# Performance work log

Measured on AMD Instinct MI355X. Metric: run time of the kernel, lower is better.

Reference implementation:

```python
import jax, jax.numpy as jnp
import numpy as np

N_NODES = 100_000
N_EDGES = 3_200_000
EPS_BN = 1e-5
EPS_NORM = 1e-12


def _sage_conv(x, src, dst, ew, pw, pb, lw, lb, rw, n_nodes):
    # project=True: relu(Linear_in->in) applied to source features
    xp = jax.nn.relu(x @ pw + pb)                       # [N, in]
    msg = xp[src] * ew[:, None]                         # [E, in] gather + weight
    agg = jax.ops.segment_sum(msg, dst, num_segments=n_nodes)      # scatter-sum
    cnt = jax.ops.segment_sum(jnp.ones_like(ew), dst, num_segments=n_nodes)
    mean = agg / jnp.maximum(cnt, 1.0)[:, None]         # scatter-mean
    out = mean @ lw + lb + x @ rw                       # neighbor lin + root lin
    # normalize=True: L2 normalize rows
    nrm = jnp.sqrt(jnp.sum(out * out, axis=-1, keepdims=True))
    return out / jnp.maximum(nrm, EPS_NORM)


def setup_inputs() -> dict:
    key = jax.random.key(0)
    ks = jax.random.split(key, 20)
    d = {}
    d["h"] = jax.random.normal(ks[0], (N_NODES, 5), dtype=jnp.float32)
    d["edge_index"] = jax.random.randint(ks[1], (2, N_EDGES), 0, N_NODES, dtype=jnp.int32)
    d["edge_weight"] = jax.random.uniform(ks[2], (N_EDGES,), dtype=jnp.float32)
    # BatchNorm1d(5) params (conv2_norm in the source is unused in forward)
    d["bn_gamma"] = jnp.ones((5,), jnp.float32)
    d["bn_beta"] = jnp.zeros((5,), jnp.float32)

    def lin(k, fan_in, fan_out):
        return jax.random.normal(k, (fan_in, fan_out), jnp.float32) * (1.0 / np.sqrt(fan_in))

    # conv1: 5 -> 64 ; conv2: 64 -> 64 (fixing source bug) ; conv3: 64 -> 5
    dims = [(5, 64), (64, 64), (64, 5)]
    ki = 3
    for i, (fi, fo) in enumerate(dims, start=1):
        d[f"c{i}_pw"] = lin(ks[ki], fi, fi); ki += 1
        d[f"c{i}_pb"] = jnp.zeros((fi,), jnp.float32)
        d[f"c{i}_lw"] = lin(ks[ki], fi, fo); ki += 1
        d[f"c{i}_lb"] = jnp.zeros((fo,), jnp.float32)
        d[f"c{i}_rw"] = lin(ks[ki], fi, fo); ki += 1
    return d


def reference(h, edge_index, edge_weight, bn_gamma, bn_beta,
              c1_pw, c1_pb, c1_lw, c1_lb, c1_rw,
              c2_pw, c2_pb, c2_lw, c2_lb, c2_rw,
              c3_pw, c3_pb, c3_lw, c3_lb, c3_rw):
    src, dst = edge_index[0], edge_index[1]
    # BatchNorm1d (training-mode batch statistics, biased variance)
    mu = jnp.mean(h, axis=0)
    var = jnp.mean((h - mu) ** 2, axis=0)
    x = (h - mu) * jax.lax.rsqrt(var + EPS_BN) * bn_gamma + bn_beta

    x = jax.nn.relu(_sage_conv(x, src, dst, edge_weight, c1_pw, c1_pb, c1_lw, c1_lb, c1_rw, N_NODES))
    x = jax.nn.relu(_sage_conv(x, src, dst, edge_weight, c2_pw, c2_pb, c2_lw, c2_lb, c2_rw, N_NODES))
    x = _sage_conv(x, src, dst, edge_weight, c3_pw, c3_pb, c3_lw, c3_lb, c3_rw, N_NODES)
    # dropout omitted (deterministic / eval-mode reference)
    return x
```

## Files before the change

### kernel.cpp

```cpp
#include <hip/hip_runtime.h>
#include <hip/hip_bf16.h>

#define N_NODES 100000
#define N_EDGES 3200000
#define BSH 8
#define NB 391

typedef __hip_bfloat16 bf16;

#define RL(v, k) __int_as_float(__builtin_amdgcn_readlane(__float_as_int(v), (k)))

__device__ __forceinline__ float loadF(const void* p, long long i, int isf32) {
    if (isf32) return ((const float*)p)[i];
    unsigned short v = ((const unsigned short*)p)[i];
    union { unsigned u; float f; } c;
    c.u = ((unsigned)v) << 16;
    return c.f;
}

__device__ __forceinline__ unsigned packEdge(int s, float w) {
    bf16 b = __float2bfloat16(w);
    unsigned short bits = *(unsigned short*)&b;
    return ((unsigned)s << 15) | (unsigned)(bits & 0x7FFF);
}
__device__ __forceinline__ int edgeSrc(unsigned u) { return (int)(u >> 15); }
__device__ __forceinline__ float edgeW(unsigned u) {
    union { unsigned x; float f; } c;
    c.x = (u & 0x7FFFu) << 16;
    return c.f;
}

#define W_GAMMA 0
#define W_BETA 8
#define W_C1PW 16
#define W_C1PB 48
#define W_C1LW 56
#define W_C1LB 376
#define W_C1RW 440
#define W_C2PW 760
#define W_C2PB 4856
#define W_C2LW 4920
#define W_C2LB 9016
#define W_C2RW 9080
#define W_C3PW 13176
#define W_C3PB 17272
#define W_C3LW 17336
#define W_C3LB 17656
#define W_C3RW 17664

__global__ void detect_dtype(const void* ew, int* flag) {
    const unsigned short* u = (const unsigned short*)ew;
    int lane = threadIdx.x;
    int big = 0;
    for (int i = lane; i < 1024; i += 64) {
        unsigned short v = u[2 * i];
        int ex = (v >> 7) & 0xFF;
        if (ex >= 128) big++;
    }
#pragma unroll
    for (int o = 32; o; o >>= 1) big += __shfl_xor(big, o, 64);
    if (lane == 0) *flag = (big > 100) ? 1 : 0;
}

__global__ void cvt_weights(const int* flag,
                            const void* p0, const void* p1, const void* p2, const void* p3,
                            const void* p4, const void* p5, const void* p6, const void* p7,
                            const void* p8, const void* p9, const void* p10, const void* p11,
                            const void* p12, const void* p13, const void* p14, const void* p15,
                            const void* p16, float* __restrict__ wts) {
    const void* ptrs[17] = {p0, p1, p2, p3, p4, p5, p6, p7, p8,
                            p9, p10, p11, p12, p13, p14, p15, p16};
    const int sz[17] = {5, 5, 25, 5, 320, 64, 320, 4096, 64,
                        4096, 64, 4096, 4096, 64, 320, 5, 320};
    const int off[17] = {W_GAMMA, W_BETA, W_C1PW, W_C1PB, W_C1LW, W_C1LB, W_C1RW,
                         W_C2PW, W_C2PB, W_C2LW, W_C2LB, W_C2RW,
                         W_C3PW, W_C3PB, W_C3LW, W_C3LB, W_C3RW};
    int t = blockIdx.x;
    int isf32 = *flag;
    for (int i = threadIdx.x; i < sz[t]; i += blockDim.x)
        wts[off[t] + i] = loadF(ptrs[t], i, isf32);
}

__global__ void bn_stats(const void* __restrict__ h, const int* __restrict__ flag,
                         float* __restrict__ stats) {
    int isf32 = *flag;
    float s[5] = {0, 0, 0, 0, 0}, q[5] = {0, 0, 0, 0, 0};
    int tid = blockIdx.x * blockDim.x + threadIdx.x;
    int stride = gridDim.x * blockDim.x;
    for (int i = tid; i < N_NODES; i += stride) {
#pragma unroll
        for (int f = 0; f < 5; f++) {
            float v = loadF(h, i * 5 + f, isf32);
            s[f] += v;
            q[f] += v * v;
        }
    }
#pragma unroll
    for (int f = 0; f < 5; f++) {
#pragma unroll
        for (int o = 32; o; o >>= 1) {
            s[f] += __shfl_xor(s[f], o, 64);
            q[f] += __shfl_xor(q[f], o, 64);
        }
    }
    __shared__ float ls[4][10];
    int wave = threadIdx.x >> 6, lane = threadIdx.x & 63;
    if (lane == 0) {
#pragma unroll
        for (int f = 0; f < 5; f++) { ls[wave][f] = s[f]; ls[wave][5 + f] = q[f]; }
    }
    __syncthreads();
    if (threadIdx.x < 10) {
        float v = ls[0][threadIdx.x] + ls[1][threadIdx.x] + ls[2][threadIdx.x] + ls[3][threadIdx.x];
        int idx = (threadIdx.x < 5) ? threadIdx.x : (threadIdx.x - 5 + 8);
        atomicAdd(&stats[idx], v);
    }
}

__global__ void bn_proj1(const void* __restrict__ h, const int* __restrict__ flag,
                         const float* __restrict__ stats, const float* __restrict__ wts,
                         float* __restrict__ xbn, float* __restrict__ xp1) {
    __shared__ float s_sc[5], s_sb[5];
    if (threadIdx.x < 5) {
        int f = threadIdx.x;
        float mean = stats[f] / (float)N_NODES;
        float var = stats[8 + f] / (float)N_NODES - mean * mean;
        float sc = wts[W_GAMMA + f] * rsqrtf(var + 1e-5f);
        s_sc[f] = sc;
        s_sb[f] = wts[W_BETA + f] - mean * sc;
    }
    __syncthreads();
    int isf32 = *flag;
    int i = blockIdx.x * blockDim.x + threadIdx.x;
    if (i >= N_NODES) return;
    float x[5];
#pragma unroll
    for (int f = 0; f < 5; f++)
        x[f] = loadF(h, i * 5 + f, isf32) * s_sc[f] + s_sb[f];
#pragma unroll
    for (int f = 0; f < 5; f++) xbn[i * 5 + f] = x[f];
#pragma unroll
    for (int j = 0; j < 5; j++) {
        float a = wts[W_C1PB + j];
#pragma unroll
        for (int k = 0; k < 5; k++) a += x[k] * wts[W_C1PW + k * 5 + j];
        xp1[i * 8 + j] = fmaxf(a, 0.f);
    }
#pragma unroll
    for (int j = 5; j < 8; j++) xp1[i * 8 + j] = 0.f;
}

__global__ void __launch_bounds__(256) bucket_hist(const int* __restrict__ dst,
                                                   int* __restrict__ bucketCnt) {
    __shared__ int hcnt[NB];
    for (int i = threadIdx.x; i < NB; i += 256) hcnt[i] = 0;
    __syncthreads();
    int per = (N_EDGES + gridDim.x - 1) / gridDim.x;
    int s = blockIdx.x * per;
    int e = min(s + per, N_EDGES);
    for (int i = s + threadIdx.x; i < e; i += 256)
        atomicAdd(&hcnt[dst[i] >> BSH], 1);
    __syncthreads();
    for (int i = threadIdx.x; i < NB; i += 256)
        if (hcnt[i]) atomicAdd(&bucketCnt[i], hcnt[i]);
}

__global__ void __launch_bounds__(512) bucket_scan(const int* __restrict__ bucketCnt,
                                                   int* __restrict__ bucketStart,
                                                   int* __restrict__ bucketCursor) {
    int tid = threadIdx.x, lane = tid & 63, w = tid >> 6;
    int v = (tid < NB) ? bucketCnt[tid] : 0;
    int sc = v;
#pragma unroll
    for (int o = 1; o < 64; o <<= 1) {
        int t = __shfl_up(sc, o, 64);
        if (lane >= o) sc += t;
    }
    __shared__ int ws[8];
    if (lane == 63) ws[w] = sc;
    __syncthreads();
    if (w == 0) {
        int wv = (lane < 8) ? ws[lane] : 0;
        int s2 = wv;
#pragma unroll
        for (int o = 1; o < 8; o <<= 1) {
            int t = __shfl_up(s2, o, 64);
            if (lane >= o) s2 += t;
        }
        if (lane < 8) ws[lane] = s2;
    }
    __syncthreads();
    int woff = w ? ws[w - 1] : 0;
    int ex = woff + sc - v;
    if (tid < NB) {
        bucketStart[tid] = ex;
        bucketCursor[tid] = ex;
    }
    if (tid == 0) bucketStart[NB] = N_EDGES;
}

__global__ void __launch_bounds__(256) bucket_stage(const int* __restrict__ src,
                                                    const int* __restrict__ dst,
                                                    const void* __restrict__ ew,
                                                    const int* __restrict__ flag,
                                                    int* __restrict__ bucketCursor,
                                                    uint2* __restrict__ stage) {
    __shared__ int hcnt[NB], cur[NB];
    int isf32 = *flag;
    for (int i = threadIdx.x; i < NB; i += 256) hcnt[i] = 0;
    __syncthreads();
    int per = (N_EDGES + gridDim.x - 1) / gridDim.x;
    int s = blockIdx.x * per;
    int e = min(s + per, N_EDGES);
    for (int i = s + threadIdx.x; i < e; i += 256)
        atomicAdd(&hcnt[dst[i] >> BSH], 1);
    __syncthreads();
    for (int i = threadIdx.x; i < NB; i += 256)
        cur[i] = hcnt[i] ? atomicAdd(&bucketCursor[i], hcnt[i]) : 0;
    __syncthreads();
    for (int i = s + threadIdx.x; i < e; i += 256) {
        int d = dst[i];
        int slot = atomicAdd(&cur[d >> BSH], 1);
        stage[slot] = make_uint2((unsigned)d, packEdge(src[i], loadF(ew, i, isf32)));
    }
}

__global__ void __launch_bounds__(256) bucket_place(const uint2* __restrict__ stage,
                                                    const int* __restrict__ bucketStart,
                                                    int* __restrict__ start,
                                                    unsigned* __restrict__ perm) {
    int b = blockIdx.x, tid = threadIdx.x;
    int base = bucketStart[b];
    int cnt = bucketStart[b + 1] - base;
    int n0 = b << BSH;
    int nn = min(256, N_NODES - n0);
    __shared__ int lcnt[256], loff[256], ws[4];
    lcnt[tid] = 0;
    __syncthreads();
    for (int i = tid; i < cnt; i += 256)
        atomicAdd(&lcnt[stage[base + i].x & 255], 1);
    __syncthreads();
    int lane = tid & 63, w = tid >> 6;
    int v = lcnt[tid];
    int sc = v;
#pragma unroll
    for (int o = 1; o < 64; o <<= 1) {
        int t = __shfl_up(sc, o, 64);
        if (lane >= o) sc += t;
    }
    if (lane == 63) ws[w] = sc;
    __syncthreads();
    int woff = 0;
    for (int k = 0; k < w; k++) woff += ws[k];
    loff[tid] = woff + sc - v;
    __syncthreads();
    if (tid < nn) start[n0 + tid] = base + loff[tid];
    if (b == 0 && tid == 0) start[N_NODES] = N_EDGES;
    lcnt[tid] = 0;
    __syncthreads();
    for (int i = tid; i < cnt; i += 256) {
        uint2 sv = stage[base + i];
        int l = sv.x & 255;
        int p = atomicAdd(&lcnt[l], 1);
        perm[base + loff[l] + p] = sv.y;
    }
}

__global__ void __launch_bounds__(256) conv1_gather(const float* __restrict__ xp1,
                                                    const float* __restrict__ xbn,
                                                    const int* __restrict__ start,
                                                    const unsigned* __restrict__ perm,
                                                    const float* __restrict__ wts,
                                                    float* __restrict__ x1) {
    int lane = threadIdx.x & 63;
    int slot = lane >> 3, f = lane & 7;
    int wid = __builtin_amdgcn_readfirstlane((blockIdx.x * blockDim.x + threadIdx.x) >> 6);
    int nw = (gridDim.x * blockDim.x) >> 6;
    float Wlw[5], Wrw[5];
#pragma unroll
    for (int k = 0; k < 5; k++) {
        Wlw[k] = wts[W_C1LW + k * 64 + lane];
        Wrw[k] = wts[W_C1RW + k * 64 + lane];
    }
    float lb = wts[W_C1LB + lane];
    for (int node = wid; node < N_NODES; node += nw) {
        int e0 = start[node], e1 = start[node + 1];
        float acc = 0.f;
        for (int eb = e0; eb < e1; eb += 32) {
            unsigned p[4];
#pragma unroll
            for (int q = 0; q < 4; q++) {
                int e = eb + q * 8 + slot;
                p[q] = (e < e1) ? perm[e] : 0u;
            }
            float v[4];
#pragma unroll
            for (int q = 0; q < 4; q++)
                v[q] = xp1[(size_t)(p[q] >> 15) * 8 + f];
#pragma unroll
            for (int q = 0; q < 4; q++)
                acc += v[q] * edgeW(p[q]);
        }
        acc += __shfl_xor(acc, 8, 64);
        acc += __shfl_xor(acc, 16, 64);
        acc += __shfl_xor(acc, 32, 64);
        float ic = 1.f / fmaxf((float)(e1 - e0), 1.f);
        float xb = (lane < 5) ? xbn[node * 5 + lane] : 0.f;
        float out = lb;
#pragma unroll
        for (int k = 0; k < 5; k++)
            out += RL(acc, k) * ic * Wlw[k] + RL(xb, k) * Wrw[k];
        float ss = out * out;
#pragma unroll
        for (int o = 32; o; o >>= 1) ss += __shfl_xor(ss, o, 64);
        float xv = fmaxf(out / fmaxf(sqrtf(ss), 1e-12f), 0.f);
        x1[(size_t)node * 64 + lane] = xv;
    }
}

__global__ void __launch_bounds__(256) proj2_blocked(const float* __restrict__ x1,
                                                     const float* __restrict__ wts,
                                                     bf16* __restrict__ y2) {
    int lane = threadIdx.x & 63;
    int wid = (blockIdx.x * blockDim.x + threadIdx.x) >> 6;
    int nb = wid * 16;
    if (nb >= N_NODES) return;
    float xv[16];
#pragma unroll
    for (int n = 0; n < 16; n++) {
        int node = nb + n;
        xv[n] = (node < N_NODES) ? x1[(size_t)node * 64 + lane] : 0.f;
    }
    float a[16];
    float pb = wts[W_C2PB + lane];
#pragma unroll
    for (int n = 0; n < 16; n++) a[n] = pb;
#pragma unroll
    for (int c = 0; c < 4; c++) {
        float Wc[16];
#pragma unroll
        for (int j = 0; j < 16; j++) Wc[j] = wts[W_C2PW + (c * 16 + j) * 64 + lane];
#pragma unroll
        for (int n = 0; n < 16; n++) {
#pragma unroll
            for (int j = 0; j < 16; j++)
                a[n] += RL(xv[n], c * 16 + j) * Wc[j];
        }
    }
#pragma unroll
    for (int n = 0; n < 16; n++) a[n] = fmaxf(a[n], 0.f);
    float b[16];
#pragma unroll
    for (int n = 0; n < 16; n++) b[n] = 0.f;
#pragma unroll
    for (int c = 0; c < 4; c++) {
        float Wc[16];
#pragma unroll
        for (int j = 0; j < 16; j++) Wc[j] = wts[W_C2LW + (c * 16 + j) * 64 + lane];
#pragma unroll
        for (int n = 0; n < 16; n++) {
#pragma unroll
            for (int j = 0; j < 16; j++)
                b[n] += RL(a[n], c * 16 + j) * Wc[j];
        }
    }
#pragma unroll
    for (int n = 0; n < 16; n++) {
        int node = nb + n;
        if (node < N_NODES) y2[(size_t)node * 64 + lane] = __float2bfloat16(b[n]);
    }
}

__global__ void __launch_bounds__(256) conv2_fused_reg(const bf16* __restrict__ y2,
                                                       const int* __restrict__ start,
                                                       const unsigned* __restrict__ perm,
                                                       const float* __restrict__ x1,
                                                       const float* __restrict__ wts,
                                                       float* __restrict__ x2) {
    int lane = threadIdx.x & 63;
    int wid = __builtin_amdgcn_readfirstlane((blockIdx.x * blockDim.x + threadIdx.x) >> 6);
    int nw = (gridDim.x * blockDim.x) >> 6;
    float W[64];
#pragma unroll
    for (int k = 0; k < 64; k++) W[k] = wts[W_C2RW + k * 64 + lane];
    float lb = wts[W_C2LB + lane];
    for (int node = wid; node < N_NODES; node += nw) {
        int e0 = start[node], e1 = start[node + 1];
        float acc = 0.f;
        int e = e0;
        for (; e + 16 <= e1; e += 16) {
            unsigned p[16];
#pragma unroll
            for (int u = 0; u < 16; u++) p[u] = perm[e + u];
            float v[16];
#pragma unroll
            for (int u = 0; u < 16; u++)
                v[u] = __bfloat162float(y2[(size_t)edgeSrc(p[u]) * 64 + lane]);
#pragma unroll
            for (int u = 0; u < 16; u++) acc += v[u] * edgeW(p[u]);
        }
        for (; e + 4 <= e1; e += 4) {
            unsigned p[4];
#pragma unroll
            for (int u = 0; u < 4; u++) p[u] = perm[e + u];
            float v[4];
#pragma unroll
            for (int u = 0; u < 4; u++)
                v[u] = __bfloat162float(y2[(size_t)edgeSrc(p[u]) * 64 + lane]);
#pragma unroll
            for (int u = 0; u < 4; u++) acc += v[u] * edgeW(p[u]);
        }
        for (; e < e1; e++) {
            unsigned p = perm[e];
            acc += __bfloat162float(y2[(size_t)edgeSrc(p) * 64 + lane]) * edgeW(p);
        }
        float ic = 1.f / fmaxf((float)(e1 - e0), 1.f);
        float xv = x1[(size_t)node * 64 + lane];
        float o0 = acc * ic + lb, o1 = 0.f, o2 = 0.f, o3 = 0.f;
#pragma unroll
        for (int k = 0; k < 64; k += 4) {
            o0 += RL(xv, k) * W[k];
            o1 += RL(xv, k + 1) * W[k + 1];
            o2 += RL(xv, k + 2) * W[k + 2];
            o3 += RL(xv, k + 3) * W[k + 3];
        }
        float out = (o0 + o1) + (o2 + o3);
        float ss = out * out;
#pragma unroll
        for (int o = 32; o; o >>= 1) ss += __shfl_xor(ss, o, 64);
        float v = out / fmaxf(sqrtf(ss), 1e-12f);
        x2[(size_t)node * 64 + lane] = fmaxf(v, 0.f);
    }
}

__global__ void __launch_bounds__(256) proj3_reg(const float* __restrict__ x2,
                                                 const float* __restrict__ wts,
                                                 float* __restrict__ y3) {
    int lane = threadIdx.x & 63;
    int wid = __builtin_amdgcn_readfirstlane((blockIdx.x * blockDim.x + threadIdx.x) >> 6);
    int nw = (gridDim.x * blockDim.x) >> 6;
    float W1[64], Wl[5];
#pragma unroll
    for (int k = 0; k < 64; k++) W1[k] = wts[W_C3PW + k * 64 + lane];
#pragma unroll
    for (int j = 0; j < 5; j++) Wl[j] = wts[W_C3LW + lane * 5 + j];
    float pb = wts[W_C3PB + lane];
    for (int node = wid; node < N_NODES; node += nw) {
        float xv = x2[(size_t)node * 64 + lane];
        float a0 = pb, a1 = 0.f, a2 = 0.f, a3 = 0.f;
#pragma unroll
        for (int k = 0; k < 64; k += 4) {
            a0 += RL(xv, k) * W1[k];
            a1 += RL(xv, k + 1) * W1[k + 1];
            a2 += RL(xv, k + 2) * W1[k + 2];
            a3 += RL(xv, k + 3) * W1[k + 3];
        }
        float xp = fmaxf((a0 + a1) + (a2 + a3), 0.f);
#pragma unroll
        for (int j = 0; j < 5; j++) {
            float p = xp * Wl[j];
#pragma unroll
            for (int o = 32; o; o >>= 1) p += __shfl_xor(p, o, 64);
            if (lane == j) y3[(size_t)node * 8 + j] = p;
        }
    }
}

__global__ void __launch_bounds__(256) conv3_fused(const float* __restrict__ y3,
                                                   const float* __restrict__ x2,
                                                   const int* __restrict__ start,
                                                   const unsigned* __restrict__ perm,
                                                   const float* __restrict__ wts,
                                                   const int* __restrict__ flag,
                                                   void* __restrict__ outp) {
    int lane = threadIdx.x & 63;
    int wid = __builtin_amdgcn_readfirstlane((blockIdx.x * blockDim.x + threadIdx.x) >> 6);
    int nw = (gridDim.x * blockDim.x) >> 6;
    float Wr[5];
#pragma unroll
    for (int j = 0; j < 5; j++) Wr[j] = wts[W_C3RW + lane * 5 + j];
    float lb3[5];
#pragma unroll
    for (int j = 0; j < 5; j++) lb3[j] = wts[W_C3LB + j];
    int isf32 = *flag;
    for (int node = wid; node < N_NODES; node += nw) {
        int e0 = start[node], e1 = start[node + 1];
        float s0 = 0, s1 = 0, s2 = 0, s3 = 0, s4 = 0;
        for (int eb = e0; eb < e1; eb += 64) {
            int e = eb + lane;
            if (e < e1) {
                unsigned p = perm[e];
                float w = edgeW(p);
                const float* row = y3 + (size_t)edgeSrc(p) * 8;
                float4 v4 = *(const float4*)row;
                float v5 = row[4];
                s0 += v4.x * w; s1 += v4.y * w; s2 += v4.z * w;
                s3 += v4.w * w; s4 += v5 * w;
            }
        }
#pragma unroll
        for (int o = 32; o; o >>= 1) {
            s0 += __shfl_xor(s0, o, 64);
            s1 += __shfl_xor(s1, o, 64);
            s2 += __shfl_xor(s2, o, 64);
            s3 += __shfl_xor(s3, o, 64);
            s4 += __shfl_xor(s4, o, 64);
        }
        float ic = 1.f / fmaxf((float)(e1 - e0), 1.f);
        float xv = x2[(size_t)node * 64 + lane];
        float m[5] = {s0 * ic, s1 * ic, s2 * ic, s3 * ic, s4 * ic};
        float r[5], ss = 0.f;
#pragma unroll
        for (int j = 0; j < 5; j++) {
            float p = xv * Wr[j];
#pragma unroll
            for (int o = 32; o; o >>= 1) p += __shfl_xor(p, o, 64);
            r[j] = p + m[j] + lb3[j];
            ss += r[j] * r[j];
        }
        float inv = 1.f / fmaxf(sqrtf(ss), 1e-12f);
#pragma unroll
        for (int j = 0; j < 5; j++) {
            if (lane == j) {
                float v = r[j] * inv;
                if (isf32) ((float*)outp)[node * 5 + j] = v;
                else ((bf16*)outp)[node * 5 + j] = __float2bfloat16(v);
            }
        }
    }
}

extern "C" void kernel_launch(void* const* d_in, const int* in_sizes, int n_in,
                              void* d_out, int out_size, void* d_ws, size_t ws_size,
                              hipStream_t stream) {
    const void* h = d_in[0];
    const int* ei = (const int*)d_in[1];
    const int* src = ei;
    const int* dst = ei + N_EDGES;
    const void* ew = d_in[2];

    float* W = (float*)d_ws;
    int* flag = (int*)W;
    float* stats = W + 16;
    float* wts = W + 64;
    float* xbn = W + 20480;
    float* xp1 = xbn + N_NODES * 5;
    int* startp = (int*)(xp1 + N_NODES * 8);
    int* bucketCnt = startp + N_NODES + 64;
    int* bucketStart = bucketCnt + NB + 1;
    int* bucketCursor = bucketStart + NB + 1;
    unsigned* perm = (unsigned*)(bucketCursor + NB + 62);
    float* x1 = (float*)(perm + N_EDGES);
    uint2* stage = (uint2*)x1;
    bf16* y2 = (bf16*)(x1 + (size_t)N_NODES * 64);
    float* x2 = x1;
    float* y3 = xp1;

    detect_dtype<<<1, 64, 0, stream>>>(ew, flag);
    cvt_weights<<<17, 256, 0, stream>>>(flag,
        d_in[3], d_in[4],
        d_in[5], d_in[6], d_in[7], d_in[8], d_in[9],
        d_in[10], d_in[11], d_in[12], d_in[13], d_in[14],
        d_in[15], d_in[16], d_in[17], d_in[18], d_in[19],
        wts);

    hipMemsetAsync(stats, 0, 32 * sizeof(float), stream);
    hipMemsetAsync(bucketCnt, 0, NB * sizeof(int), stream);

    bn_stats<<<200, 256, 0, stream>>>(h, flag, stats);
    bn_proj1<<<(N_NODES + 255) / 256, 256, 0, stream>>>(h, flag, stats, wts, xbn, xp1);

    bucket_hist<<<512, 256, 0, stream>>>(dst, bucketCnt);
    bucket_scan<<<1, 512, 0, stream>>>(bucketCnt, bucketStart, bucketCursor);
    bucket_stage<<<512, 256, 0, stream>>>(src, dst, ew, flag, bucketCursor, stage);
    bucket_place<<<NB, 256, 0, stream>>>(stage, bucketStart, startp, perm);

    conv1_gather<<<4096, 256, 0, stream>>>(xp1, xbn, startp, perm, wts, x1);
    proj2_blocked<<<(N_NODES / 16 + 1 + 3) / 4, 256, 0, stream>>>(x1, wts, y2);

    conv2_fused_reg<<<4096, 256, 0, stream>>>(y2, startp, perm, x1, wts, x2);

    proj3_reg<<<2048, 256, 0, stream>>>(x2, wts, y3);
    conv3_fused<<<2048, 256, 0, stream>>>(y3, x2, startp, perm, wts, flag, d_out);
}
```

Measured before the change: 558.9 us.

## Sort edges by source and gather conv2 in source-range phases with grid barriers

Adds a kernel that bitonic-sorts each node's packed edge list by source index and records per-node boundaries for four source-ID quarters. The conv2 gather then runs as a persistent-style kernel of 1024 blocks that process one source quarter at a time, separated by global atomic spin barriers, accumulating partial sums in shared memory. The goal is to keep the working set of y2 rows cache-resident during each phase and so cut random-gather traffic. The cost is an extra sort pass, grid-wide barriers that depend on all blocks being co-resident (there is a timeout fallback), and lower occupancy from the launch bounds and shared-memory use.

```diff
diff --git a/kernel.cpp b/kernel.cpp
--- a/kernel.cpp
+++ b/kernel.cpp
@@ -5,6 +5,8 @@
 #define N_EDGES 3200000
 #define BSH 8
 #define NB 391
+#define CNBLK 1024
+#define NPB 100
 
 typedef __hip_bfloat16 bf16;
 
@@ -266,6 +268,46 @@
     }
 }
 
+__global__ void __launch_bounds__(256) sort_perm(const int* __restrict__ start,
+                                                 unsigned* __restrict__ perm,
+                                                 ushort4* __restrict__ cums) {
+    int lane = threadIdx.x & 63;
+    int wid = (blockIdx.x * blockDim.x + threadIdx.x) >> 6;
+    int nw = (gridDim.x * blockDim.x) >> 6;
+    for (int node = wid; node < N_NODES; node += nw) {
+        int e0 = start[node], e1 = start[node + 1];
+        int deg = e1 - e0;
+        if (deg > 64) {
+            if (lane == 0)
+                cums[node] = make_ushort4((unsigned short)deg, (unsigned short)deg,
+                                          (unsigned short)deg, (unsigned short)deg);
+            continue;
+        }
+        unsigned v = (lane < deg) ? perm[e0 + lane] : 0xFFFFFFFFu;
+#pragma unroll
+        for (int k = 2; k <= 64; k <<= 1) {
+#pragma unroll
+            for (int j = k >> 1; j > 0; j >>= 1) {
+                unsigned o = __shfl_xor(v, j, 64);
+                bool asc = ((lane & k) == 0);
+                bool lower = ((lane & j) == 0);
+                unsigned mn = min(v, o), mx = max(v, o);
+                v = (asc == lower) ? mn : mx;
+            }
+        }
+        if (lane < deg) perm[e0 + lane] = v;
+        int srcn = (int)(v >> 15);
+        bool valid = (lane < deg);
+        int ph = (srcn >= 25000) + (srcn >= 50000) + (srcn >= 75000);
+        unsigned long long b0 = __ballot(valid && ph <= 0);
+        unsigned long long b1 = __ballot(valid && ph <= 1);
+        unsigned long long b2 = __ballot(valid && ph <= 2);
+        if (lane == 0)
+            cums[node] = make_ushort4((unsigned short)__popcll(b0), (unsigned short)__popcll(b1),
+                                      (unsigned short)__popcll(b2), (unsigned short)deg);
+    }
+}
+
 __global__ void __launch_bounds__(256) conv1_gather(const float* __restrict__ xp1,
                                                     const float* __restrict__ xbn,
                                                     const int* __restrict__ start,
@@ -371,50 +413,75 @@
     }
 }
 
-__global__ void __launch_bounds__(256) conv2_fused_reg(const bf16* __restrict__ y2,
-                                                       const int* __restrict__ start,
-                                                       const unsigned* __restrict__ perm,
-                                                       const float* __restrict__ x1,
-                                                       const float* __restrict__ wts,
-                                                       float* __restrict__ x2) {
-    int lane = threadIdx.x & 63;
-    int wid = __builtin_amdgcn_readfirstlane((blockIdx.x * blockDim.x + threadIdx.x) >> 6);
-    int nw = (gridDim.x * blockDim.x) >> 6;
+__global__ void __launch_bounds__(256, 4) conv2_coop(const bf16* __restrict__ y2,
+                                                     const int* __restrict__ start,
+                                                     const unsigned* __restrict__ perm,
+                                                     const ushort4* __restrict__ cums,
+                                                     const float* __restrict__ x1,
+                                                     const float* __restrict__ wts,
+                                                     float* __restrict__ x2,
+                                                     int* __restrict__ bar) {
+    __shared__ float sacc[NPB * 64];
+    int tid = threadIdx.x, lane = tid & 63, w = tid >> 6;
+    int nb0 = blockIdx.x * NPB;
+    for (int i = tid; i < NPB * 64; i += 256) sacc[i] = 0.f;
+    __syncthreads();
+#pragma unroll
+    for (int p = 0; p < 4; p++) {
+        for (int i = w; i < NPB; i += 4) {
+            int node = nb0 + i;
+            if (node >= N_NODES) break;
+            int e0 = start[node];
+            ushort4 c = cums[node];
+            int lo = (p == 0) ? 0 : ((p == 1) ? c.x : ((p == 2) ? c.y : c.z));
+            int hi = (p == 0) ? c.x : ((p == 1) ? c.y : ((p == 2) ? c.z : c.w));
+            int e = e0 + lo, eh = e0 + hi;
+            float a = 0.f;
+            for (; e + 8 <= eh; e += 8) {
+                unsigned pk[8];
+#pragma unroll
+                for (int u = 0; u < 8; u++) pk[u] = perm[e + u];
+                float vv[8];
+#pragma unroll
+                for (int u = 0; u < 8; u++)
+                    vv[u] = __bfloat162float(y2[(size_t)(pk[u] >> 15) * 64 + lane]);
+#pragma unroll
+                for (int u = 0; u < 8; u++) a += vv[u] * edgeW(pk[u]);
+            }
+            for (; e + 2 <= eh; e += 2) {
+                unsigned pa = perm[e], pb2 = perm[e + 1];
+                float va = __bfloat162float(y2[(size_t)(pa >> 15) * 64 + lane]);
+                float vb = __bfloat162float(y2[(size_t)(pb2 >> 15) * 64 + lane]);
+                a += va * edgeW(pa) + vb * edgeW(pb2);
+            }
+            for (; e < eh; e++) {
+                unsigned pp = perm[e];
+                a += __bfloat162float(y2[(size_t)(pp >> 15) * 64 + lane]) * edgeW(pp);
+            }
+            sacc[i * 64 + lane] += a;
+        }
+        if (p < 3) {
+            __syncthreads();
+            if (tid == 0) {
+                __hip_atomic_fetch_add(&bar[p], 1, __ATOMIC_ACQ_REL, __HIP_MEMORY_SCOPE_AGENT);
+                int it = 0;
+                while (__hip_atomic_load(&bar[p], __ATOMIC_ACQUIRE, __HIP_MEMORY_SCOPE_AGENT) < CNBLK
+                       && ++it < 5000)
+                    __builtin_amdgcn_s_sleep(8);
+            }
+            __syncthreads();
+        }
+    }
     float W[64];
 #pragma unroll
     for (int k = 0; k < 64; k++) W[k] = wts[W_C2RW + k * 64 + lane];
     float lb = wts[W_C2LB + lane];
-    for (int node = wid; node < N_NODES; node += nw) {
-        int e0 = start[node], e1 = start[node + 1];
-        float acc = 0.f;
-        int e = e0;
-        for (; e + 16 <= e1; e += 16) {
-            unsigned p[16];
-#pragma unroll
-            for (int u = 0; u < 16; u++) p[u] = perm[e + u];
-            float v[16];
-#pragma unroll
-            for (int u = 0; u < 16; u++)
-                v[u] = __bfloat162float(y2[(size_t)edgeSrc(p[u]) * 64 + lane]);
-#pragma unroll
-            for (int u = 0; u < 16; u++) acc += v[u] * edgeW(p[u]);
-        }
-        for (; e + 4 <= e1; e += 4) {
-            unsigned p[4];
-#pragma unroll
-            for (int u = 0; u < 4; u++) p[u] = perm[e + u];
-            float v[4];
-#pragma unroll
-            for (int u = 0; u < 4; u++)
-                v[u] = __bfloat162float(y2[(size_t)edgeSrc(p[u]) * 64 + lane]);
-#pragma unroll
-            for (int u = 0; u < 4; u++) acc += v[u] * edgeW(p[u]);
-        }
-        for (; e < e1; e++) {
-            unsigned p = perm[e];
-            acc += __bfloat162float(y2[(size_t)edgeSrc(p) * 64 + lane]) * edgeW(p);
-        }
-        float ic = 1.f / fmaxf((float)(e1 - e0), 1.f);
+    for (int i = w; i < NPB; i += 4) {
+        int node = nb0 + i;
+        if (node >= N_NODES) break;
+        int deg = start[node + 1] - start[node];
+        float acc = sacc[i * 64 + lane];
+        float ic = 1.f / fmaxf((float)deg, 1.f);
         float xv = x1[(size_t)node * 64 + lane];
         float o0 = acc * ic + lb, o1 = 0.f, o2 = 0.f, o3 = 0.f;
 #pragma unroll
@@ -555,6 +622,8 @@
     bf16* y2 = (bf16*)(x1 + (size_t)N_NODES * 64);
     float* x2 = x1;
     float* y3 = xp1;
+    ushort4* cums = (ushort4*)(y2 + (size_t)N_NODES * 64);
+    int* bar = (int*)(cums + N_NODES);
 
     detect_dtype<<<1, 64, 0, stream>>>(ew, flag);
     cvt_weights<<<17, 256, 0, stream>>>(flag,
@@ -566,6 +635,7 @@
 
     hipMemsetAsync(stats, 0, 32 * sizeof(float), stream);
     hipMemsetAsync(bucketCnt, 0, NB * sizeof(int), stream);
+    hipMemsetAsync(bar, 0, 16 * sizeof(int), stream);
 
     bn_stats<<<200, 256, 0, stream>>>(h, flag, stats);
     bn_proj1<<<(N_NODES + 255) / 256, 256, 0, stream>>>(h, flag, stats, wts, xbn, xp1);
@@ -575,10 +645,12 @@
     bucket_stage<<<512, 256, 0, stream>>>(src, dst, ew, flag, bucketCursor, stage);
     bucket_place<<<NB, 256, 0, stream>>>(stage, bucketStart, startp, perm);
 
+    sort_perm<<<2048, 256, 0, stream>>>(startp, perm, cums);
+
     conv1_gather<<<4096, 256, 0, stream>>>(xp1, xbn, startp, perm, wts, x1);
     proj2_blocked<<<(N_NODES / 16 + 1 + 3) / 4, 256, 0, stream>>>(x1, wts, y2);
 
-    conv2_fused_reg<<<4096, 256, 0, stream>>>(y2, startp, perm, x1, wts, x2);
+    conv2_coop<<<CNBLK, 256, 0, stream>>>(y2, startp, perm, cums, x1, wts, x2, bar);
 
     proj3_reg<<<2048, 256, 0, stream>>>(x2, wts, y3);
     conv3_fused<<<2048, 256, 0, stream>>>(y3, x2, startp, perm, wts, flag, d_out);
```

Measured after the change: 1.397 ms. 2.5x slower.
